# Optimization experiments

Hardware: AMD Instinct MI355X
Metric: run time of the kernel (lower is better)

## Reference

```python
import jax, jax.numpy as jnp
from jax import lax
import numpy as np

NUM_CLASSES = 85742  # MS1M-scale classifier
C = 512              # feature channels
KH = KW = 1          # 1x1 conv classifier kernel
B = 512              # batch size
H = W = 7            # feature map spatial size


def setup_inputs() -> dict:
    key = jax.random.key(0)
    kx, kw = jax.random.split(key)
    x = jax.random.normal(kx, (B, C, H, W), dtype=jnp.float32)
    # labels: all distinct so torch's labels.unique() has deterministic size B
    labels = jnp.arange(B, dtype=jnp.int64)
    weight = jax.random.normal(kw, (NUM_CLASSES, C, KH, KW), dtype=jnp.float32) * 0.02
    bias = jnp.zeros((NUM_CLASSES,), dtype=jnp.float32)  # requires_grad=False in torch
    return {"x": x, "labels": labels, "weight": weight, "bias": bias}


def reference(x, labels, weight, bias):
    # Partial-FC style: gather the unique-label subset of the classifier weight,
    # then run a conv producing logits only over that subset.
    # jnp.unique with static size=B is jit-compatible; labels are all distinct here.
    labels_unique = jnp.unique(labels, size=labels.shape[0], fill_value=0)  # [U], sorted
    w_sub = weight[labels_unique]   # [U, C, KH, KW] irregular gather
    b_sub = bias[labels_unique]     # [U]
    logits = lax.conv_general_dilated(
        x, w_sub,
        window_strides=(1, 1), padding="VALID",
        dimension_numbers=("NCHW", "OIHW", "NCHW"),
    )  # [B, U, H, W]
    return logits + b_sub[None, :, None, None]
```

## Files before the change

kernel.cpp:

```cpp
#include <hip/hip_runtime.h>
#include <hip/hip_bf16.h>

#define CIN    512
#define BATCH  512
#define HW     49
#define UDIM   512
#define MTOT   (BATCH * HW)
#define MT     128
#define NMB    (MTOT / MT)
#define UHALF  256
#define KT     16
#define NSTEP  (CIN / KT)
#define NBLK   (NMB * 2)

typedef short  bf16x8 __attribute__((ext_vector_type(8)));
typedef short  s16x4  __attribute__((ext_vector_type(4)));
typedef short  s16x8  __attribute__((ext_vector_type(8)));
typedef float  f32x4  __attribute__((ext_vector_type(4)));
typedef float  f32x16 __attribute__((ext_vector_type(16)));

#define MFMA32(A, B, C) __builtin_amdgcn_mfma_f32_32x32x16_bf16((A), (B), (C), 0, 0, 0)

__device__ __forceinline__ void split2(float v, unsigned short& h, unsigned short& l) {
  unsigned int b  = __float_as_uint(v);
  unsigned int hb = (b + 0x7FFFu + ((b >> 16) & 1u)) >> 16;
  float hf        = __uint_as_float(hb << 16);
  unsigned int lb = __float_as_uint(v - hf);
  h = (unsigned short)hb;
  l = (unsigned short)((lb + 0x7FFFu + ((lb >> 16) & 1u)) >> 16);
}

__device__ __forceinline__ f32x16 zero16() {
  f32x16 r;
#pragma unroll
  for (int i = 0; i < 16; ++i) r[i] = 0.f;
  return r;
}

__global__ __launch_bounds__(512, 4) void convcls_fused(
    const float* __restrict__ x,
    const int*   __restrict__ labels,
    const float* __restrict__ weight,
    const float* __restrict__ bias,
    float*       __restrict__ out)
{
  __shared__ __attribute__((aligned(16))) unsigned short WhB[2][2][UHALF][8];
  __shared__ __attribute__((aligned(16))) unsigned short WlB[2][2][UHALF][8];
  __shared__ __attribute__((aligned(16))) unsigned short XhB[2][2][MT][8];
  __shared__ __attribute__((aligned(16))) unsigned short XlB[2][2][MT][8];
  __shared__ int   sl[BATCH];
  __shared__ int   lblr[UHALF];
  __shared__ float bsubs[UHALF];

  const int bid = blockIdx.x;
  const int swz = (bid & 7) * (NBLK / 8) + (bid >> 3);
  const int uh  = swz / NMB;
  const int mb  = swz - uh * NMB;

  const int tid  = threadIdx.x;
  const int wave = tid >> 6, lane = tid & 63;
  const int l31  = lane & 31, lq = lane >> 5;

  {
    const int stride = (labels[1] == 0) ? 2 : 1;
    const int lt = labels[tid * stride];
    sl[tid] = lt;
    __syncthreads();
    int rank = 0;
#pragma unroll 8
    for (int j = 0; j < BATCH; ++j) rank += (sl[j] < lt) ? 1 : 0;
    const int rloc = rank - uh * UHALF;
    if ((unsigned)rloc < UHALF) { lblr[rloc] = lt; bsubs[rloc] = bias[lt]; }
    __syncthreads();
  }

  const int uloc = tid & 255;
  const int kq   = tid >> 8;
  const float* wp = weight + (size_t)lblr[uloc] * CIN + kq * 8;
  const int mloc = tid & 127;
  const int ks   = tid >> 7;
  const int kqs  = ks >> 1;
  const int j0   = (ks & 1) * 4;
  const int mg   = mb * MT + mloc;
  const int bimg = mg / HW;
  const int hwp  = mg - bimg * HW;
  const float* xsrc = x + (size_t)bimg * (CIN * HW) + hwp;

  f32x16 a00 = zero16(), a01 = zero16(), a10 = zero16(), a11 = zero16();
  const int uoff = (wave & 3) * 64;
  const int moff = (wave >> 2) * 64;

  {
    f32x4 w0 = *(const f32x4*)(wp);
    f32x4 w1 = *(const f32x4*)(wp + 4);
    float xv[4];
#pragma unroll
    for (int i = 0; i < 4; ++i) xv[i] = xsrc[(size_t)(ks * 4 + i) * HW];
    s16x8 ph, pl;
#pragma unroll
    for (int i = 0; i < 4; ++i) {
      unsigned short h, l;
      split2(w0[i], h, l); ph[i] = (short)h;     pl[i] = (short)l;
      split2(w1[i], h, l); ph[4 + i] = (short)h; pl[4 + i] = (short)l;
    }
    *(s16x8*)&WhB[0][kq][uloc][0] = ph;
    *(s16x8*)&WlB[0][kq][uloc][0] = pl;
    s16x4 qh, ql;
#pragma unroll
    for (int i = 0; i < 4; ++i) {
      unsigned short h, l; split2(xv[i], h, l);
      qh[i] = (short)h; ql[i] = (short)l;
    }
    *(s16x4*)&XhB[0][kqs][mloc][j0] = qh;
    *(s16x4*)&XlB[0][kqs][mloc][j0] = ql;
  }
  __syncthreads();

  for (int s = 0; s < NSTEP; ++s) {
    const int cur = s & 1, nxt = cur ^ 1;
    const bool pf = (s + 1 < NSTEP);
    f32x4 w0, w1;
    float xv[4];
    if (pf) {
      const float* wps = wp + (size_t)(s + 1) * KT;
      w0 = *(const f32x4*)(wps);
      w1 = *(const f32x4*)(wps + 4);
      const float* xs = xsrc + (size_t)(s + 1) * KT * HW;
#pragma unroll
      for (int i = 0; i < 4; ++i) xv[i] = xs[(size_t)(ks * 4 + i) * HW];
    }

    bf16x8 ah0 = *(const bf16x8*)&WhB[cur][lq][uoff + l31][0];
    bf16x8 ah1 = *(const bf16x8*)&WhB[cur][lq][uoff + 32 + l31][0];
    bf16x8 al0 = *(const bf16x8*)&WlB[cur][lq][uoff + l31][0];
    bf16x8 al1 = *(const bf16x8*)&WlB[cur][lq][uoff + 32 + l31][0];
    bf16x8 bh0 = *(const bf16x8*)&XhB[cur][lq][moff + l31][0];
    bf16x8 bh1 = *(const bf16x8*)&XhB[cur][lq][moff + 32 + l31][0];
    bf16x8 bl0 = *(const bf16x8*)&XlB[cur][lq][moff + l31][0];
    bf16x8 bl1 = *(const bf16x8*)&XlB[cur][lq][moff + 32 + l31][0];

    a00 = MFMA32(ah0, bh0, a00);  a01 = MFMA32(ah0, bh1, a01);
    a10 = MFMA32(ah1, bh0, a10);  a11 = MFMA32(ah1, bh1, a11);
    a00 = MFMA32(ah0, bl0, a00);  a01 = MFMA32(ah0, bl1, a01);
    a10 = MFMA32(ah1, bl0, a10);  a11 = MFMA32(ah1, bl1, a11);
    a00 = MFMA32(al0, bh0, a00);  a01 = MFMA32(al0, bh1, a01);
    a10 = MFMA32(al1, bh0, a10);  a11 = MFMA32(al1, bh1, a11);

    if (pf) {
      s16x8 ph, pl;
#pragma unroll
      for (int i = 0; i < 4; ++i) {
        unsigned short h, l;
        split2(w0[i], h, l); ph[i] = (short)h;     pl[i] = (short)l;
        split2(w1[i], h, l); ph[4 + i] = (short)h; pl[4 + i] = (short)l;
      }
      *(s16x8*)&WhB[nxt][kq][uloc][0] = ph;
      *(s16x8*)&WlB[nxt][kq][uloc][0] = pl;
      s16x4 qh, ql;
#pragma unroll
      for (int i = 0; i < 4; ++i) {
        unsigned short h, l; split2(xv[i], h, l);
        qh[i] = (short)h; ql[i] = (short)l;
      }
      *(s16x4*)&XhB[nxt][kqs][mloc][j0] = qh;
      *(s16x4*)&XlB[nxt][kqs][mloc][j0] = ql;
    }
    __syncthreads();
  }

  const int u0g = uh * UHALF + uoff;
  const int m0g = mb * MT + moff;
  const int mA  = m0g + l31,      mB = m0g + 32 + l31;
  const int bA  = mA / HW,        hA = mA - bA * HW;
  const int bB  = mB / HW,        hB = mB - bB * HW;
  float* oA = out + (size_t)bA * (UDIM * HW) + hA;
  float* oB = out + (size_t)bB * (UDIM * HW) + hB;
#pragma unroll
  for (int r = 0; r < 16; ++r) {
    const int urow = (r & 3) + 8 * (r >> 2) + 4 * lq;
    {
      const int ul = uoff + urow;
      const float bs = bsubs[ul];
      const int u = u0g + urow;
      oA[(size_t)u * HW] = a00[r] + bs;
      oB[(size_t)u * HW] = a01[r] + bs;
    }
    {
      const int ul = uoff + 32 + urow;
      const float bs = bsubs[ul];
      const int u = u0g + 32 + urow;
      oA[(size_t)u * HW] = a10[r] + bs;
      oB[(size_t)u * HW] = a11[r] + bs;
    }
  }
}

extern "C" void kernel_launch(void* const* d_in, const int* in_sizes, int n_in,
                              void* d_out, int out_size, void* d_ws, size_t ws_size,
                              hipStream_t stream)
{
  const float* x      = (const float*)d_in[0];
  const int*   labels = (const int*)d_in[1];
  const float* weight = (const float*)d_in[2];
  const float* bias   = (const float*)d_in[3];
  float*       out    = (float*)d_out;

  convcls_fused<<<NBLK, 512, 0, stream>>>(x, labels, weight, bias, out);
}
```

Measured before the change: 328.4 us.

## Pre-split gathered weights into bf16 hi/lo workspace and stream via global_load_lds

Moves the label ranking, weight gather and the fp32-to-bf16 hi/lo split into a separate prep kernel that writes a pre-tiled weight layout into workspace. The main kernel then loads weight tiles straight into LDS with global_load_lds instead of recomputing splits in every block. It also halves the M tile to 64 with 256 threads per block, which doubles the number of blocks. The cost is an extra launch and workspace traffic, and the weight tiles are now reused over fewer output rows per block.

```diff
diff --git a/kernel.cpp b/kernel.cpp
--- a/kernel.cpp
+++ b/kernel.cpp
@@ -6,7 +6,7 @@
 #define HW     49
 #define UDIM   512
 #define MTOT   (BATCH * HW)
-#define MT     128
+#define MT     64
 #define NMB    (MTOT / MT)
 #define UHALF  256
 #define KT     16
@@ -15,11 +15,15 @@
 
 typedef short  bf16x8 __attribute__((ext_vector_type(8)));
 typedef short  s16x4  __attribute__((ext_vector_type(4)));
-typedef short  s16x8  __attribute__((ext_vector_type(8)));
-typedef float  f32x4  __attribute__((ext_vector_type(4)));
 typedef float  f32x16 __attribute__((ext_vector_type(16)));
 
 #define MFMA32(A, B, C) __builtin_amdgcn_mfma_f32_32x32x16_bf16((A), (B), (C), 0, 0, 0)
+
+__device__ __forceinline__ void gload_lds16(const void* g, void* l) {
+  __builtin_amdgcn_global_load_lds(
+      (const __attribute__((address_space(1))) void*)g,
+      (__attribute__((address_space(3))) void*)l, 16, 0, 0);
+}
 
 __device__ __forceinline__ void split2(float v, unsigned short& h, unsigned short& l) {
   unsigned int b  = __float_as_uint(v);
@@ -37,20 +41,53 @@
   return r;
 }
 
-__global__ __launch_bounds__(512, 4) void convcls_fused(
+__global__ void wprep(const int* __restrict__ labels,
+                      const float* __restrict__ weight,
+                      const float* __restrict__ bias,
+                      unsigned short* __restrict__ whi,
+                      unsigned short* __restrict__ wlo,
+                      float* __restrict__ bsub)
+{
+  __shared__ int sl[BATCH];
+  __shared__ int myl;
+  const int u   = blockIdx.x;
+  const int tid = threadIdx.x;
+  const int stride = (labels[1] == 0) ? 2 : 1;
+  sl[tid]       = labels[tid * stride];
+  sl[tid + 256] = labels[(tid + 256) * stride];
+  __syncthreads();
+#pragma unroll
+  for (int t = 0; t < 2; ++t) {
+    const int lt = sl[tid + t * 256];
+    int rank = 0;
+#pragma unroll 8
+    for (int j = 0; j < BATCH; ++j) rank += (sl[j] < lt) ? 1 : 0;
+    if (rank == u) { myl = lt; bsub[u] = bias[lt]; }
+  }
+  __syncthreads();
+  const int lbl = myl;
+  const float* wrow = weight + (size_t)lbl * CIN;
+  for (int k = tid; k < CIN; k += 256) {
+    unsigned short h, l;
+    split2(wrow[k], h, l);
+    const int s = k >> 4, kq = (k >> 3) & 1, j = k & 7;
+    const size_t idx = (((size_t)(s * 2 + kq)) * UDIM + u) * 8 + j;
+    whi[idx] = h;
+    wlo[idx] = l;
+  }
+}
+
+__global__ __launch_bounds__(256, 4) void convcls_main(
     const float* __restrict__ x,
-    const int*   __restrict__ labels,
-    const float* __restrict__ weight,
-    const float* __restrict__ bias,
-    float*       __restrict__ out)
+    const unsigned short* __restrict__ whi,
+    const unsigned short* __restrict__ wlo,
+    const float* __restrict__ bsub,
+    float* __restrict__ out)
 {
   __shared__ __attribute__((aligned(16))) unsigned short WhB[2][2][UHALF][8];
   __shared__ __attribute__((aligned(16))) unsigned short WlB[2][2][UHALF][8];
   __shared__ __attribute__((aligned(16))) unsigned short XhB[2][2][MT][8];
   __shared__ __attribute__((aligned(16))) unsigned short XlB[2][2][MT][8];
-  __shared__ int   sl[BATCH];
-  __shared__ int   lblr[UHALF];
-  __shared__ float bsubs[UHALF];
 
   const int bid = blockIdx.x;
   const int swz = (bid & 7) * (NBLK / 8) + (bid >> 3);
@@ -61,24 +98,8 @@
   const int wave = tid >> 6, lane = tid & 63;
   const int l31  = lane & 31, lq = lane >> 5;
 
-  {
-    const int stride = (labels[1] == 0) ? 2 : 1;
-    const int lt = labels[tid * stride];
-    sl[tid] = lt;
-    __syncthreads();
-    int rank = 0;
-#pragma unroll 8
-    for (int j = 0; j < BATCH; ++j) rank += (sl[j] < lt) ? 1 : 0;
-    const int rloc = rank - uh * UHALF;
-    if ((unsigned)rloc < UHALF) { lblr[rloc] = lt; bsubs[rloc] = bias[lt]; }
-    __syncthreads();
-  }
-
-  const int uloc = tid & 255;
-  const int kq   = tid >> 8;
-  const float* wp = weight + (size_t)lblr[uloc] * CIN + kq * 8;
-  const int mloc = tid & 127;
-  const int ks   = tid >> 7;
+  const int mloc = tid & 63;
+  const int ks   = tid >> 6;
   const int kqs  = ks >> 1;
   const int j0   = (ks & 1) * 4;
   const int mg   = mb * MT + mloc;
@@ -87,24 +108,23 @@
   const float* xsrc = x + (size_t)bimg * (CIN * HW) + hwp;
 
   f32x16 a00 = zero16(), a01 = zero16(), a10 = zero16(), a11 = zero16();
-  const int uoff = (wave & 3) * 64;
-  const int moff = (wave >> 2) * 64;
+  const int uoff = wave * 64;
 
   {
-    f32x4 w0 = *(const f32x4*)(wp);
-    f32x4 w1 = *(const f32x4*)(wp + 4);
+#pragma unroll
+    for (int i = 0; i < 4; ++i) {
+      const int chunk = wave * 4 + i;
+      const bool hi = chunk < 8;
+      const int c8 = chunk & 7, kqc = c8 >> 2, qc = c8 & 3;
+      const unsigned short* g = (hi ? whi : wlo)
+          + (size_t)kqc * (UDIM * 8) + (uh * UHALF + qc * 64) * 8 + lane * 8;
+      char* l = (char*)(hi ? &WhB[0][0][0][0] : &WlB[0][0][0][0])
+          + kqc * 4096 + qc * 1024;
+      gload_lds16(g, l);
+    }
     float xv[4];
 #pragma unroll
     for (int i = 0; i < 4; ++i) xv[i] = xsrc[(size_t)(ks * 4 + i) * HW];
-    s16x8 ph, pl;
-#pragma unroll
-    for (int i = 0; i < 4; ++i) {
-      unsigned short h, l;
-      split2(w0[i], h, l); ph[i] = (short)h;     pl[i] = (short)l;
-      split2(w1[i], h, l); ph[4 + i] = (short)h; pl[4 + i] = (short)l;
-    }
-    *(s16x8*)&WhB[0][kq][uloc][0] = ph;
-    *(s16x8*)&WlB[0][kq][uloc][0] = pl;
     s16x4 qh, ql;
 #pragma unroll
     for (int i = 0; i < 4; ++i) {
@@ -119,12 +139,20 @@
   for (int s = 0; s < NSTEP; ++s) {
     const int cur = s & 1, nxt = cur ^ 1;
     const bool pf = (s + 1 < NSTEP);
-    f32x4 w0, w1;
     float xv[4];
     if (pf) {
-      const float* wps = wp + (size_t)(s + 1) * KT;
-      w0 = *(const f32x4*)(wps);
-      w1 = *(const f32x4*)(wps + 4);
+      const size_t so = (size_t)(s + 1) * (2 * UDIM * 8);
+#pragma unroll
+      for (int i = 0; i < 4; ++i) {
+        const int chunk = wave * 4 + i;
+        const bool hi = chunk < 8;
+        const int c8 = chunk & 7, kqc = c8 >> 2, qc = c8 & 3;
+        const unsigned short* g = (hi ? whi : wlo) + so
+            + (size_t)kqc * (UDIM * 8) + (uh * UHALF + qc * 64) * 8 + lane * 8;
+        char* l = (char*)(hi ? &WhB[nxt][0][0][0] : &WlB[nxt][0][0][0])
+            + kqc * 4096 + qc * 1024;
+        gload_lds16(g, l);
+      }
       const float* xs = xsrc + (size_t)(s + 1) * KT * HW;
 #pragma unroll
       for (int i = 0; i < 4; ++i) xv[i] = xs[(size_t)(ks * 4 + i) * HW];
@@ -134,10 +162,10 @@
     bf16x8 ah1 = *(const bf16x8*)&WhB[cur][lq][uoff + 32 + l31][0];
     bf16x8 al0 = *(const bf16x8*)&WlB[cur][lq][uoff + l31][0];
     bf16x8 al1 = *(const bf16x8*)&WlB[cur][lq][uoff + 32 + l31][0];
-    bf16x8 bh0 = *(const bf16x8*)&XhB[cur][lq][moff + l31][0];
-    bf16x8 bh1 = *(const bf16x8*)&XhB[cur][lq][moff + 32 + l31][0];
-    bf16x8 bl0 = *(const bf16x8*)&XlB[cur][lq][moff + l31][0];
-    bf16x8 bl1 = *(const bf16x8*)&XlB[cur][lq][moff + 32 + l31][0];
+    bf16x8 bh0 = *(const bf16x8*)&XhB[cur][lq][l31][0];
+    bf16x8 bh1 = *(const bf16x8*)&XhB[cur][lq][32 + l31][0];
+    bf16x8 bl0 = *(const bf16x8*)&XlB[cur][lq][l31][0];
+    bf16x8 bl1 = *(const bf16x8*)&XlB[cur][lq][32 + l31][0];
 
     a00 = MFMA32(ah0, bh0, a00);  a01 = MFMA32(ah0, bh1, a01);
     a10 = MFMA32(ah1, bh0, a10);  a11 = MFMA32(ah1, bh1, a11);
@@ -147,15 +175,6 @@
     a10 = MFMA32(al1, bh0, a10);  a11 = MFMA32(al1, bh1, a11);
 
     if (pf) {
-      s16x8 ph, pl;
-#pragma unroll
-      for (int i = 0; i < 4; ++i) {
-        unsigned short h, l;
-        split2(w0[i], h, l); ph[i] = (short)h;     pl[i] = (short)l;
-        split2(w1[i], h, l); ph[4 + i] = (short)h; pl[4 + i] = (short)l;
-      }
-      *(s16x8*)&WhB[nxt][kq][uloc][0] = ph;
-      *(s16x8*)&WlB[nxt][kq][uloc][0] = pl;
       s16x4 qh, ql;
 #pragma unroll
       for (int i = 0; i < 4; ++i) {
@@ -169,7 +188,7 @@
   }
 
   const int u0g = uh * UHALF + uoff;
-  const int m0g = mb * MT + moff;
+  const int m0g = mb * MT;
   const int mA  = m0g + l31,      mB = m0g + 32 + l31;
   const int bA  = mA / HW,        hA = mA - bA * HW;
   const int bB  = mB / HW,        hB = mB - bB * HW;
@@ -179,16 +198,14 @@
   for (int r = 0; r < 16; ++r) {
     const int urow = (r & 3) + 8 * (r >> 2) + 4 * lq;
     {
-      const int ul = uoff + urow;
-      const float bs = bsubs[ul];
       const int u = u0g + urow;
+      const float bs = bsub[u];
       oA[(size_t)u * HW] = a00[r] + bs;
       oB[(size_t)u * HW] = a01[r] + bs;
     }
     {
-      const int ul = uoff + 32 + urow;
-      const float bs = bsubs[ul];
       const int u = u0g + 32 + urow;
+      const float bs = bsub[u];
       oA[(size_t)u * HW] = a10[r] + bs;
       oB[(size_t)u * HW] = a11[r] + bs;
     }
@@ -205,5 +222,10 @@
   const float* bias   = (const float*)d_in[3];
   float*       out    = (float*)d_out;
 
-  convcls_fused<<<NBLK, 512, 0, stream>>>(x, labels, weight, bias, out);
-}
+  unsigned short* whi  = (unsigned short*)d_ws;
+  unsigned short* wlo  = (unsigned short*)((char*)d_ws + 512 * 1024);
+  float*          bsub = (float*)((char*)d_ws + 1024 * 1024);
+
+  wprep<<<UDIM, 256, 0, stream>>>(labels, weight, bias, whi, wlo, bsub);
+  convcls_main<<<NBLK, 256, 0, stream>>>(x, whi, wlo, bsub, out);
+}
```

Measured after the change: 307.1 us. 6.5% less time.
